# Kernel tuning notes

Hardware: AMD Instinct MI355X
Metric: run time of the kernel (lower is better)

The kernel has to match this reference:

```python
import jax, jax.numpy as jnp
import numpy as np
from jax import lax

EPS = 1e-5
ALPHA = 100.0

def leaky_relu(x):
    return jnp.where(x >= 0, x, 0.2 * x)

def instance_norm(x):
    # per-sample, per-channel over (H, W), affine=False, eps=1e-5
    m = jnp.mean(x, axis=(2, 3), keepdims=True)
    v = jnp.var(x, axis=(2, 3), keepdims=True)
    return (x - m) / jnp.sqrt(v + EPS)

def conv2d(x, W, b, stride=1):
    y = lax.conv_general_dilated(x, W, (stride, stride), 'VALID',
                                 dimension_numbers=('NCHW', 'OIHW', 'NCHW'))
    return y + b[None, :, None, None]

def leaky_conv(x, W, b, pad, stride):
    # ReflectionPad2d(pad) -> Conv2d(pad=0) -> InstanceNorm -> LeakyReLU(0.2)
    if pad > 0:
        x = jnp.pad(x, ((0, 0), (0, 0), (pad, pad), (pad, pad)), mode='reflect')
    y = conv2d(x, W, b, stride)
    return leaky_relu(instance_norm(y))

def up2x_align_corners(x):
    # nn.UpsamplingBilinear2d(scale_factor=2) == bilinear with align_corners=True
    n, c, H, W = x.shape
    def coords(S):
        pos = jnp.arange(2 * S, dtype=x.dtype) * (S - 1) / (2 * S - 1)
        i0 = jnp.floor(pos).astype(jnp.int32)
        i1 = jnp.minimum(i0 + 1, S - 1)
        return i0, i1, pos - i0
    i0, i1, fh = coords(H)
    x = x[:, :, i0, :] * (1 - fh)[None, None, :, None] + x[:, :, i1, :] * fh[None, None, :, None]
    j0, j1, fw = coords(W)
    x = x[:, :, :, j0] * (1 - fw) + x[:, :, :, j1] * fw
    return x

def upsample_block(x, W, b):
    x = up2x_align_corners(x)
    # Conv2d(3,3,k=3,s=1,p=1) uses ZERO padding (plain nn.Conv2d padding arg)
    x = jnp.pad(x, ((0, 0), (0, 0), (1, 1), (1, 1)))
    return leaky_relu(instance_norm(conv2d(x, W, b)))

def cal_correlation(fa, fb, alpha):
    n, c, h, w = fa.shape
    fa = fa - jnp.mean(fa, axis=(2, 3), keepdims=True)
    fb = fb - jnp.mean(fb, axis=(2, 3), keepdims=True)
    fa = fa.reshape(n, c, h * w)
    fb = fb.reshape(n, c, h * w)
    fa = fa / (jnp.linalg.norm(fa, axis=1, keepdims=True) + EPS)
    fb = fb / (jnp.linalg.norm(fb, axis=1, keepdims=True) + EPS)
    energy = jnp.einsum('ncp,ncq->npq', fb, fa) * alpha  # [n, hw_b, hw_a]
    return jax.nn.softmax(energy, axis=1)

def setup_inputs() -> dict:
    key = jax.random.key(0)
    ks = jax.random.split(key, 16)
    C = 256
    d = {
        'fa_raw': jax.random.normal(ks[0], (2, C, 64, 64), jnp.float32),
        'fb_raw': jax.random.normal(ks[1], (2, C, 64, 64), jnp.float32),
        'fc_raw': jax.random.normal(ks[2], (2, 3, 256, 256), jnp.float32),
        'Wa': jax.random.normal(ks[3], (C // 4, C, 1, 1), jnp.float32) * 0.05,
        'ba': jnp.zeros((C // 4,), jnp.float32),
        'Wb': jax.random.normal(ks[4], (C // 4, C, 1, 1), jnp.float32) * 0.05,
        'bb': jnp.zeros((C // 4,), jnp.float32),
        'Wc1': jax.random.normal(ks[5], (3, 3, 3, 3), jnp.float32) * 0.2,
        'bc1': jnp.zeros((3,), jnp.float32),
        'Wc2': jax.random.normal(ks[6], (3, 3, 3, 3), jnp.float32) * 0.2,
        'bc2': jnp.zeros((3,), jnp.float32),
        'Wu1': jax.random.normal(ks[7], (3, 3, 3, 3), jnp.float32) * 0.2,
        'bu1': jnp.zeros((3,), jnp.float32),
        'Wu2': jax.random.normal(ks[8], (3, 3, 3, 3), jnp.float32) * 0.2,
        'bu2': jnp.zeros((3,), jnp.float32),
    }
    return d

def reference(fa_raw, fb_raw, fc_raw, Wa, ba, Wb, bb, Wc1, bc1, Wc2, bc2, Wu1, bu1, Wu2, bu2):
    fa = leaky_conv(fa_raw, Wa, ba, pad=0, stride=1)          # [n, 64, 64, 64]
    fb = leaky_conv(fb_raw, Wb, bb, pad=0, stride=1)
    fc = leaky_conv(fc_raw, Wc1, bc1, pad=1, stride=2)        # [n, 3, 128, 128]
    fc = leaky_conv(fc, Wc2, bc2, pad=1, stride=2)            # [n, 3, 64, 64]
    corr_ab_T = cal_correlation(fa, fb, ALPHA)                # [n, 4096, 4096]
    n, c, h, w = fc.shape
    fc_warp = jnp.einsum('ncp,npq->ncq', fc.reshape(n, c, h * w), corr_ab_T)
    fc_warp = fc_warp.reshape(n, c, h, w)
    fc_warp = upsample_block(fc_warp, Wu1, bu1)               # [n, 3, 128, 128]
    fc_warp = upsample_block(fc_warp, Wu2, bu2)               # [n, 3, 256, 256]
    return fc_warp, corr_ab_T
```

## Files before the change

kernel.cpp:

```cpp
#include <hip/hip_runtime.h>
#include <math.h>

#define EPS 1e-5f

typedef short short8 __attribute__((ext_vector_type(8)));
typedef __bf16 bf16x8 __attribute__((ext_vector_type(8)));
typedef float f32x4  __attribute__((ext_vector_type(4)));

__device__ __forceinline__ float lrelu(float x){ return x >= 0.f ? x : 0.2f*x; }

__device__ __forceinline__ short f2bf_s(float x){
    unsigned u = __float_as_uint(x);
    unsigned r = (u + 0x7FFFu + ((u >> 16) & 1u)) >> 16;
    return (short)r;
}
__device__ __forceinline__ float bfs2f(short h){
    return __uint_as_float(((unsigned)(unsigned short)h) << 16);
}

__device__ __forceinline__ f32x4 mfma16(bf16x8 a, bf16x8 b, f32x4 c){
    return __builtin_amdgcn_mfma_f32_16x16x32_bf16(a, b, c, 0, 0, 0);
}

__global__ __launch_bounds__(256,2) void feat_conv(
    const float* __restrict__ fa_raw, const float* __restrict__ fb_raw,
    const float* __restrict__ Wa, const float* __restrict__ Wb,
    const float* __restrict__ ba, const float* __restrict__ bb,
    float* __restrict__ Y, float* __restrict__ FSUM)
{
    __shared__ float wS[256*65];
    __shared__ float xS[16*64];

    int blk = blockIdx.x;
    int pch = blk & 63, n = (blk>>6)&1, side = blk>>7;
    int p0 = pch*64;
    const float* x    = (side ? fb_raw : fa_raw) + (size_t)n*256*4096 + p0;
    const float* W    = side ? Wb : Wa;
    const float* bias = side ? bb : ba;
    int tid = threadIdx.x;

    #pragma unroll
    for (int it=0; it<64; it++){
        int idx = it*256 + tid;
        int co = idx >> 8, ci = idx & 255;
        wS[ci*65 + co] = W[idx];
    }

    int pl = tid & 63, cog = tid >> 6;
    float acc[16];
    #pragma unroll
    for (int j=0;j<16;j++) acc[j] = 0.f;

    for (int cb=0; cb<16; cb++){
        __syncthreads();
        #pragma unroll
        for (int it=0; it<4; it++){
            int idx = it*256 + tid;
            int cl = idx >> 6, pp = idx & 63;
            xS[idx] = x[(size_t)(cb*16+cl)*4096 + pp];
        }
        __syncthreads();
        #pragma unroll
        for (int cl=0; cl<16; cl++){
            float xr = xS[cl*64 + pl];
            const float* wr = &wS[(cb*16+cl)*65 + cog*16];
            #pragma unroll
            for (int j=0;j<16;j++) acc[j] = fmaf(xr, wr[j], acc[j]);
        }
    }

    int pair = side*2 + n;
    #pragma unroll
    for (int j=0;j<16;j++){
        acc[j] += bias[cog*16+j];
        float v = acc[j], v2 = v*v;
        #pragma unroll
        for (int off=1; off<64; off<<=1){
            v  += __shfl_xor(v,  off);
            v2 += __shfl_xor(v2, off);
        }
        if (pl == 0){
            atomicAdd(&FSUM[(pair*64 + cog*16 + j)*2],   v);
            atomicAdd(&FSUM[(pair*64 + cog*16 + j)*2+1], v2);
        }
    }

    float* yr = Y + ((size_t)pair*4096 + p0 + pl)*64 + cog*16;
    #pragma unroll
    for (int j4=0;j4<4;j4++)
        *(float4*)(yr + j4*4) = make_float4(acc[j4*4],acc[j4*4+1],acc[j4*4+2],acc[j4*4+3]);
}

__global__ __launch_bounds__(256) void feat_apply(
    float* __restrict__ Y, const float* __restrict__ FSUM, float* __restrict__ M2SUM)
{
    __shared__ float red[256];
    int tid = threadIdx.x;
    size_t base = (size_t)blockIdx.x*4096;
    int pair = (int)(base >> 18);
    int co = tid & 63;
    int ch = pair*64 + co;
    float m   = FSUM[ch*2]   * (1.f/4096.f);
    float var = FSUM[ch*2+1] * (1.f/4096.f) - m*m;
    float inv = rsqrtf(var + EPS);
    float asum = 0.f;
    #pragma unroll
    for (int it=0; it<16; it++){
        size_t idx = base + it*256 + tid;
        float y2 = lrelu((Y[idx]-m)*inv);
        Y[idx] = y2;
        asum += y2;
    }
    red[tid] = asum; __syncthreads();
    if (tid < 64)
        atomicAdd(&M2SUM[pair*64 + tid], red[tid]+red[tid+64]+red[tid+128]+red[tid+192]);
}

__global__ void feat_finish(const float* __restrict__ Y, const float* __restrict__ M2SUM,
                            short* __restrict__ PK)
{
    int r = blockIdx.x*256 + threadIdx.x;
    int pair = r >> 12;
    int p = r & 4095;
    const float4* m4 = (const float4*)(M2SUM + pair*64);
    const float4* r4 = (const float4*)(Y + (size_t)r*64);
    float s = 0.f;
    float4 v[16];
    #pragma unroll
    for (int i=0;i<16;i++){
        float4 t = r4[i], mm = m4[i];
        t.x -= mm.x*(1.f/4096.f); t.y -= mm.y*(1.f/4096.f);
        t.z -= mm.z*(1.f/4096.f); t.w -= mm.w*(1.f/4096.f);
        v[i] = t;
        s += t.x*t.x + t.y*t.y + t.z*t.z + t.w*t.w;
    }
    float inv = 1.f/(sqrtf(s)+EPS);
    #pragma unroll
    for (int i=0;i<16;i++){ v[i].x*=inv; v[i].y*=inv; v[i].z*=inv; v[i].w*=inv; }

    int qb = p >> 7, rr = p & 127, g = rr >> 4, rl = rr & 15;
    short* blk = PK + (((size_t)pair*32 + qb) << 14);
    #pragma unroll
    for (int c=0;c<8;c++){
        float x[8] = {v[2*c].x, v[2*c].y, v[2*c].z, v[2*c].w,
                      v[2*c+1].x, v[2*c+1].y, v[2*c+1].z, v[2*c+1].w};
        short8 h, l;
        #pragma unroll
        for (int j=0;j<8;j++){
            short hh = f2bf_s(x[j]);
            h[j] = hh;
            l[j] = f2bf_s(x[j] - bfs2f(hh));
        }
        int idx = g*128 + c*16 + rl;
        *(short8*)(blk + idx*8)        = h;
        *(short8*)(blk + 8192 + idx*8) = l;
    }
}

template<int STRIDE, bool REFLECT>
__global__ void conv3_kernel(const float* __restrict__ in_, int H, int Wd,
                             const float* __restrict__ wgt,
                             const float* __restrict__ bias,
                             float* __restrict__ out, float* __restrict__ sums)
{
    int oH = (H-1)/STRIDE + 1, oW = (Wd-1)/STRIDE + 1;
    int tid = threadIdx.x;
    size_t idx = (size_t)blockIdx.x*256 + tid;
    int ow = (int)(idx % oW); size_t t = idx / oW;
    int oh = (int)(t % oH); t /= oH;
    int co = (int)(t % 3); int n = (int)(t/3);
    float w[27];
    #pragma unroll
    for (int i=0;i<27;i++) w[i] = wgt[co*27 + i];
    float acc = bias[co];
    #pragma unroll
    for (int ci=0;ci<3;ci++){
        size_t base = ((size_t)(n*3+ci))*H*Wd;
        #pragma unroll
        for (int kh=0;kh<3;kh++){
            int ih = oh*STRIDE + kh - 1;
            if (REFLECT) ih = ih<0 ? -ih : (ih>=H ? 2*H-2-ih : ih);
            #pragma unroll
            for (int kw=0;kw<3;kw++){
                int iw = ow*STRIDE + kw - 1;
                if (REFLECT) iw = iw<0 ? -iw : (iw>=Wd ? 2*Wd-2-iw : iw);
                bool ok = REFLECT || (ih>=0 && ih<H && iw>=0 && iw<Wd);
                if (ok) acc += w[(ci*3+kh)*3+kw] * in_[base + (size_t)ih*Wd + iw];
            }
        }
    }
    out[idx] = acc;
    __shared__ float red[256];
    red[tid] = acc; __syncthreads();
    for (int o=128;o>0;o>>=1){ if(tid<o) red[tid]+=red[tid+o]; __syncthreads(); }
    float blockSum = red[0]; __syncthreads();
    red[tid] = acc*acc; __syncthreads();
    for (int o=128;o>0;o>>=1){ if(tid<o) red[tid]+=red[tid+o]; __syncthreads(); }
    if (tid==0){
        int pair = n*3+co;
        atomicAdd(&sums[pair*2],   blockSum);
        atomicAdd(&sums[pair*2+1], red[0]);
    }
}

template<int H>
__global__ __launch_bounds__(256) void upconv3_kernel(
    const float* __restrict__ in_, const float* __restrict__ wgt,
    const float* __restrict__ bias, float* __restrict__ out,
    float* __restrict__ sums)
{
    const int oH = 2*H;
    int tid = threadIdx.x;
    size_t idx = (size_t)blockIdx.x*256 + tid;
    int ow = (int)(idx % oH); size_t t = idx / oH;
    int oh = (int)(t % oH); t /= oH;
    int co = (int)(t % 3); int n = (int)(t/3);

    float w[27];
    #pragma unroll
    for (int i=0;i<27;i++) w[i] = wgt[co*27 + i];

    int i0[3], i1[3], j0[3], j1[3];
    float fh[3], fw[3];
    bool vh[3], vw[3];
    #pragma unroll
    for (int k=0;k<3;k++){
        int ih = oh + k - 1;
        vh[k] = (ih>=0 && ih<oH);
        int ihc = vh[k] ? ih : 0;
        float ph = (float)ihc * (float)(H-1) / (float)(oH-1);
        i0[k] = (int)ph; i1[k] = min(i0[k]+1, H-1); fh[k] = ph - (float)i0[k];
        int iw = ow + k - 1;
        vw[k] = (iw>=0 && iw<oH);
        int iwc = vw[k] ? iw : 0;
        float pw = (float)iwc * (float)(H-1) / (float)(oH-1);
        j0[k] = (int)pw; j1[k] = min(j0[k]+1, H-1); fw[k] = pw - (float)j0[k];
    }

    float acc = bias[co];
    #pragma unroll
    for (int ci=0;ci<3;ci++){
        const float* p = in_ + ((size_t)(n*3+ci))*H*H;
        #pragma unroll
        for (int kh=0;kh<3;kh++){
            if (!vh[kh]) continue;
            const float* r0 = p + (size_t)i0[kh]*H;
            const float* r1 = p + (size_t)i1[kh]*H;
            #pragma unroll
            for (int kw=0;kw<3;kw++){
                if (!vw[kw]) continue;
                float v00=r0[j0[kw]], v01=r0[j1[kw]];
                float v10=r1[j0[kw]], v11=r1[j1[kw]];
                float v0 = v00 + (v01-v00)*fw[kw];
                float v1 = v10 + (v11-v10)*fw[kw];
                float u  = v0 + (v1-v0)*fh[kh];
                acc += w[(ci*3+kh)*3+kw] * u;
            }
        }
    }
    out[idx] = acc;
    __shared__ float red[256];
    red[tid] = acc; __syncthreads();
    for (int o=128;o>0;o>>=1){ if(tid<o) red[tid]+=red[tid+o]; __syncthreads(); }
    float blockSum = red[0]; __syncthreads();
    red[tid] = acc*acc; __syncthreads();
    for (int o=128;o>0;o>>=1){ if(tid<o) red[tid]+=red[tid+o]; __syncthreads(); }
    if (tid==0){
        int pair = n*3+co;
        atomicAdd(&sums[pair*2],   blockSum);
        atomicAdd(&sums[pair*2+1], red[0]);
    }
}

__global__ void inapply_kernel(const float* __restrict__ in, const float* __restrict__ sums,
                               int planeSize, float cntInv, float* __restrict__ out)
{
    size_t idx = (size_t)blockIdx.x*256 + threadIdx.x;
    int pair = (int)(idx / planeSize);
    float m = sums[pair*2]*cntInv;
    float v = sums[pair*2+1]*cntInv - m*m;
    float inv = rsqrtf(v + EPS);
    out[idx] = lrelu((in[idx]-m)*inv);
}

template<int PASS>
__global__ __launch_bounds__(256,2) void corr_mfma(
    const short* __restrict__ PK,
    float* __restrict__ corr, float* __restrict__ SSUM,
    const float* __restrict__ fc, float* __restrict__ WARP)
{
    __shared__ short lds[32768];

    int blk = blockIdx.x;
    int qb = blk & 31, pb = (blk >> 5) & 31, n = blk >> 10;
    int tid = threadIdx.x;

    const short* pkB = PK + (((size_t)(2+n)*32 + pb) << 14);
    const short* pkA = PK + (((size_t)( n )*32 + qb) << 14);
    #pragma unroll
    for (int it=0; it<16; it++){
        int cid = it*256 + tid;
        int side = cid >> 11;
        int off  = (cid & 2047)*8;
        short8 vv = *(const short8*)((side ? pkA : pkB) + off);
        *(short8*)(lds + side*16384 + off) = vv;
    }
    __syncthreads();

    int wave = tid >> 6, lane = tid & 63;
    int wp = wave >> 1, wq = wave & 1;
    int quad = lane >> 4, l16 = lane & 15;

    f32x4 acc[4][4];
    #pragma unroll
    for (int pt=0;pt<4;pt++)
        #pragma unroll
        for (int qt=0;qt<4;qt++)
            acc[pt][qt] = (f32x4){0.f,0.f,0.f,0.f};

    #pragma unroll
    for (int kc=0;kc<2;kc++){
        int cc = kc*4 + quad;
        bf16x8 Ah[4], Al[4], Bh[4], Bl[4];
        #pragma unroll
        for (int t4=0;t4<4;t4++){
            int offA = (((wp*4+t4)*8 + cc)*16 + l16)*8;
            Ah[t4] = (bf16x8)(*(const short8*)(lds + offA));
            Al[t4] = (bf16x8)(*(const short8*)(lds + 8192 + offA));
            int offB = 16384 + (((wq*4+t4)*8 + cc)*16 + l16)*8;
            Bh[t4] = (bf16x8)(*(const short8*)(lds + offB));
            Bl[t4] = (bf16x8)(*(const short8*)(lds + 8192 + offB));
        }
        #pragma unroll
        for (int pt=0;pt<4;pt++)
            #pragma unroll
            for (int qt=0;qt<4;qt++){
                acc[pt][qt] = mfma16(Ah[pt], Bh[qt], acc[pt][qt]);
                acc[pt][qt] = mfma16(Ah[pt], Bl[qt], acc[pt][qt]);
                acc[pt][qt] = mfma16(Al[pt], Bh[qt], acc[pt][qt]);
            }
    }

    if (PASS == 0){
        float colsum[4] = {0.f,0.f,0.f,0.f};
        #pragma unroll
        for (int pt=0;pt<4;pt++)
            #pragma unroll
            for (int qt=0;qt<4;qt++)
                #pragma unroll
                for (int i=0;i<4;i++)
                    colsum[qt] += __expf(fmaf(acc[pt][qt][i], 100.f, -64.f));
        #pragma unroll
        for (int qt=0;qt<4;qt++){
            float v = colsum[qt];
            v += __shfl_xor(v, 16);
            v += __shfl_xor(v, 32);
            if (lane < 16)
                atomicAdd(&SSUM[n*4096 + qb*128 + wq*64 + qt*16 + lane], v);
        }
    } else {
        float inv4[4];
        int qoff = n*4096 + qb*128 + wq*64 + l16;
        #pragma unroll
        for (int qt=0;qt<4;qt++) inv4[qt] = 1.f / SSUM[qoff + qt*16];
        float wa0[4]={0,0,0,0}, wa1[4]={0,0,0,0}, wa2[4]={0,0,0,0};
        const float* fcb = fc + (size_t)n*12288;
        float* corrN = corr + (size_t)n*4096*4096;
        #pragma unroll
        for (int pt=0;pt<4;pt++){
            #pragma unroll
            for (int i=0;i<4;i++){
                int p = pb*128 + wp*64 + pt*16 + quad*4 + i;
                float f0 = fcb[p], f1 = fcb[4096+p], f2 = fcb[8192+p];
                float* rowp = corrN + (size_t)p*4096 + qb*128 + wq*64 + l16;
                #pragma unroll
                for (int qt=0;qt<4;qt++){
                    float u = __expf(fmaf(acc[pt][qt][i], 100.f, -64.f)) * inv4[qt];
                    __builtin_nontemporal_store(u, &rowp[qt*16]);
                    wa0[qt] += f0*u; wa1[qt] += f1*u; wa2[qt] += f2*u;
                }
            }
        }
        #pragma unroll
        for (int qt=0;qt<4;qt++){
            float v0 = wa0[qt], v1 = wa1[qt], v2 = wa2[qt];
            v0 += __shfl_xor(v0,16); v0 += __shfl_xor(v0,32);
            v1 += __shfl_xor(v1,16); v1 += __shfl_xor(v1,32);
            v2 += __shfl_xor(v2,16); v2 += __shfl_xor(v2,32);
            if (lane < 16){
                int q = qb*128 + wq*64 + qt*16 + lane;
                atomicAdd(&WARP[(size_t)n*12288 +        q], v0);
                atomicAdd(&WARP[(size_t)n*12288 + 4096 + q], v1);
                atomicAdd(&WARP[(size_t)n*12288 + 8192 + q], v2);
            }
        }
    }
}

extern "C" void kernel_launch(void* const* d_in, const int* in_sizes, int n_in,
                              void* d_out, int out_size, void* d_ws, size_t ws_size,
                              hipStream_t stream)
{
    const float* fa_raw = (const float*)d_in[0];
    const float* fb_raw = (const float*)d_in[1];
    const float* fc_raw = (const float*)d_in[2];
    const float* Wa  = (const float*)d_in[3];
    const float* ba  = (const float*)d_in[4];
    const float* Wb  = (const float*)d_in[5];
    const float* bb  = (const float*)d_in[6];
    const float* Wc1 = (const float*)d_in[7];
    const float* bc1 = (const float*)d_in[8];
    const float* Wc2 = (const float*)d_in[9];
    const float* bc2 = (const float*)d_in[10];
    const float* Wu1 = (const float*)d_in[11];
    const float* bu1 = (const float*)d_in[12];
    const float* Wu2 = (const float*)d_in[13];
    const float* bu2 = (const float*)d_in[14];

    float* ws    = (float*)d_ws;
    float* FEAT  = ws;
    float* CONV1 = FEAT  + 1048576;
    float* FC64  = CONV1 + 98304;
    float* CONV2 = FC64  + 24576;
    float* CONV3 = CONV2 + 98304;
    float* SSUM  = CONV3 + 393216;
    float* SUMS  = SSUM  + 8192;
    float* FSUM  = SUMS  + 48;
    float* M2SUM = FSUM  + 512;
    float* WARP  = M2SUM + 256;
    short* PK    = (short*)(WARP + 24576);

    float* out_fc   = (float*)d_out;
    float* out_corr = out_fc + 393216;

    hipMemsetAsync(SSUM, 0, (size_t)(8192 + 48 + 512 + 256 + 24576)*sizeof(float), stream);

    feat_conv<<<256,256,0,stream>>>(fa_raw, fb_raw, Wa, Wb, ba, bb, FEAT, FSUM);
    feat_apply<<<256,256,0,stream>>>(FEAT, FSUM, M2SUM);
    feat_finish<<<64,256,0,stream>>>(FEAT, M2SUM, PK);

    conv3_kernel<2,true><<<384,256,0,stream>>>(fc_raw, 256,256, Wc1, bc1, CONV1, SUMS+0);
    inapply_kernel<<<384,256,0,stream>>>(CONV1, SUMS+0, 16384, 1.f/16384.f, CONV1);
    conv3_kernel<2,true><<<96,256,0,stream>>>(CONV1, 128,128, Wc2, bc2, FC64, SUMS+12);
    inapply_kernel<<<96,256,0,stream>>>(FC64, SUMS+12, 4096, 1.f/4096.f, FC64);

    corr_mfma<0><<<2048,256,0,stream>>>(PK, out_corr, SSUM, FC64, WARP);
    corr_mfma<1><<<2048,256,0,stream>>>(PK, out_corr, SSUM, FC64, WARP);

    upconv3_kernel<64><<<384,256,0,stream>>>(WARP, Wu1, bu1, CONV2, SUMS+24);
    inapply_kernel<<<384,256,0,stream>>>(CONV2, SUMS+24, 16384, 1.f/16384.f, CONV2);

    upconv3_kernel<128><<<1536,256,0,stream>>>(CONV2, Wu2, bu2, CONV3, SUMS+36);
    inapply_kernel<<<1536,256,0,stream>>>(CONV3, SUMS+36, 65536, 1.f/65536.f, out_fc);
}
```

Baseline: 365.3 us.

## Fuse pre- and post-correlation stages into persistent kernels with grid barriers

Merges the feature 1x1 conv, instance-norm apply, centering and normalization/packing, and the fc conv chain into a single persistent kernel. That kernel synchronizes through software grid barriers on a global counter, and the FEAT intermediate round trip through memory goes away. The separate normalize passes are folded into the consumer convolutions and the corr kernel, and the two upsample convs plus the final apply become one barrier-synchronized kernel. This cuts launch count and memory traffic. In exchange it depends on every block being co-resident (512 blocks at 2 per CU, 768 at 3 per CU), or the barriers deadlock, and it adds spin-wait cost.

```diff
diff --git a/kernel.cpp b/kernel.cpp
--- a/kernel.cpp
+++ b/kernel.cpp
@@ -22,150 +22,28 @@
     return __builtin_amdgcn_mfma_f32_16x16x32_bf16(a, b, c, 0, 0, 0);
 }
 
-__global__ __launch_bounds__(256,2) void feat_conv(
-    const float* __restrict__ fa_raw, const float* __restrict__ fb_raw,
-    const float* __restrict__ Wa, const float* __restrict__ Wb,
-    const float* __restrict__ ba, const float* __restrict__ bb,
-    float* __restrict__ Y, float* __restrict__ FSUM)
-{
-    __shared__ float wS[256*65];
-    __shared__ float xS[16*64];
-
-    int blk = blockIdx.x;
-    int pch = blk & 63, n = (blk>>6)&1, side = blk>>7;
-    int p0 = pch*64;
-    const float* x    = (side ? fb_raw : fa_raw) + (size_t)n*256*4096 + p0;
-    const float* W    = side ? Wb : Wa;
-    const float* bias = side ? bb : ba;
-    int tid = threadIdx.x;
-
-    #pragma unroll
-    for (int it=0; it<64; it++){
-        int idx = it*256 + tid;
-        int co = idx >> 8, ci = idx & 255;
-        wS[ci*65 + co] = W[idx];
-    }
-
-    int pl = tid & 63, cog = tid >> 6;
-    float acc[16];
-    #pragma unroll
-    for (int j=0;j<16;j++) acc[j] = 0.f;
-
-    for (int cb=0; cb<16; cb++){
-        __syncthreads();
-        #pragma unroll
-        for (int it=0; it<4; it++){
-            int idx = it*256 + tid;
-            int cl = idx >> 6, pp = idx & 63;
-            xS[idx] = x[(size_t)(cb*16+cl)*4096 + pp];
-        }
-        __syncthreads();
-        #pragma unroll
-        for (int cl=0; cl<16; cl++){
-            float xr = xS[cl*64 + pl];
-            const float* wr = &wS[(cb*16+cl)*65 + cog*16];
-            #pragma unroll
-            for (int j=0;j<16;j++) acc[j] = fmaf(xr, wr[j], acc[j]);
-        }
-    }
-
-    int pair = side*2 + n;
-    #pragma unroll
-    for (int j=0;j<16;j++){
-        acc[j] += bias[cog*16+j];
-        float v = acc[j], v2 = v*v;
-        #pragma unroll
-        for (int off=1; off<64; off<<=1){
-            v  += __shfl_xor(v,  off);
-            v2 += __shfl_xor(v2, off);
-        }
-        if (pl == 0){
-            atomicAdd(&FSUM[(pair*64 + cog*16 + j)*2],   v);
-            atomicAdd(&FSUM[(pair*64 + cog*16 + j)*2+1], v2);
-        }
-    }
-
-    float* yr = Y + ((size_t)pair*4096 + p0 + pl)*64 + cog*16;
-    #pragma unroll
-    for (int j4=0;j4<4;j4++)
-        *(float4*)(yr + j4*4) = make_float4(acc[j4*4],acc[j4*4+1],acc[j4*4+2],acc[j4*4+3]);
-}
-
-__global__ __launch_bounds__(256) void feat_apply(
-    float* __restrict__ Y, const float* __restrict__ FSUM, float* __restrict__ M2SUM)
-{
-    __shared__ float red[256];
-    int tid = threadIdx.x;
-    size_t base = (size_t)blockIdx.x*4096;
-    int pair = (int)(base >> 18);
-    int co = tid & 63;
-    int ch = pair*64 + co;
-    float m   = FSUM[ch*2]   * (1.f/4096.f);
-    float var = FSUM[ch*2+1] * (1.f/4096.f) - m*m;
-    float inv = rsqrtf(var + EPS);
-    float asum = 0.f;
-    #pragma unroll
-    for (int it=0; it<16; it++){
-        size_t idx = base + it*256 + tid;
-        float y2 = lrelu((Y[idx]-m)*inv);
-        Y[idx] = y2;
-        asum += y2;
-    }
-    red[tid] = asum; __syncthreads();
-    if (tid < 64)
-        atomicAdd(&M2SUM[pair*64 + tid], red[tid]+red[tid+64]+red[tid+128]+red[tid+192]);
-}
-
-__global__ void feat_finish(const float* __restrict__ Y, const float* __restrict__ M2SUM,
-                            short* __restrict__ PK)
-{
-    int r = blockIdx.x*256 + threadIdx.x;
-    int pair = r >> 12;
-    int p = r & 4095;
-    const float4* m4 = (const float4*)(M2SUM + pair*64);
-    const float4* r4 = (const float4*)(Y + (size_t)r*64);
-    float s = 0.f;
-    float4 v[16];
-    #pragma unroll
-    for (int i=0;i<16;i++){
-        float4 t = r4[i], mm = m4[i];
-        t.x -= mm.x*(1.f/4096.f); t.y -= mm.y*(1.f/4096.f);
-        t.z -= mm.z*(1.f/4096.f); t.w -= mm.w*(1.f/4096.f);
-        v[i] = t;
-        s += t.x*t.x + t.y*t.y + t.z*t.z + t.w*t.w;
-    }
-    float inv = 1.f/(sqrtf(s)+EPS);
-    #pragma unroll
-    for (int i=0;i<16;i++){ v[i].x*=inv; v[i].y*=inv; v[i].z*=inv; v[i].w*=inv; }
-
-    int qb = p >> 7, rr = p & 127, g = rr >> 4, rl = rr & 15;
-    short* blk = PK + (((size_t)pair*32 + qb) << 14);
-    #pragma unroll
-    for (int c=0;c<8;c++){
-        float x[8] = {v[2*c].x, v[2*c].y, v[2*c].z, v[2*c].w,
-                      v[2*c+1].x, v[2*c+1].y, v[2*c+1].z, v[2*c+1].w};
-        short8 h, l;
-        #pragma unroll
-        for (int j=0;j<8;j++){
-            short hh = f2bf_s(x[j]);
-            h[j] = hh;
-            l[j] = f2bf_s(x[j] - bfs2f(hh));
-        }
-        int idx = g*128 + c*16 + rl;
-        *(short8*)(blk + idx*8)        = h;
-        *(short8*)(blk + 8192 + idx*8) = l;
-    }
-}
-
-template<int STRIDE, bool REFLECT>
-__global__ void conv3_kernel(const float* __restrict__ in_, int H, int Wd,
-                             const float* __restrict__ wgt,
-                             const float* __restrict__ bias,
-                             float* __restrict__ out, float* __restrict__ sums)
+__device__ __forceinline__ void gbar(unsigned* cnt, unsigned target){
+    __syncthreads();
+    if (threadIdx.x == 0){
+        __threadfence();
+        __hip_atomic_fetch_add(cnt, 1u, __ATOMIC_ACQ_REL, __HIP_MEMORY_SCOPE_AGENT);
+        while (__hip_atomic_load(cnt, __ATOMIC_ACQUIRE, __HIP_MEMORY_SCOPE_AGENT) < target)
+            __builtin_amdgcn_s_sleep(8);
+        __threadfence();
+    }
+    __syncthreads();
+}
+
+template<int STRIDE, bool REFLECT, bool NORM>
+__device__ __forceinline__ void conv3_unit(
+    int u, const float* __restrict__ in_, int H, int Wd,
+    const float* __restrict__ wgt, const float* __restrict__ bias,
+    const float* __restrict__ nsum, float cntInv,
+    float* __restrict__ out, float* __restrict__ sums, float* red)
 {
     int oH = (H-1)/STRIDE + 1, oW = (Wd-1)/STRIDE + 1;
     int tid = threadIdx.x;
-    size_t idx = (size_t)blockIdx.x*256 + tid;
+    size_t idx = (size_t)u*256 + tid;
     int ow = (int)(idx % oW); size_t t = idx / oW;
     int oh = (int)(t % oH); t /= oH;
     int co = (int)(t % 3); int n = (int)(t/3);
@@ -175,6 +53,13 @@
     float acc = bias[co];
     #pragma unroll
     for (int ci=0;ci<3;ci++){
+        float mm = 0.f, iv = 0.f;
+        if (NORM){
+            int pr = n*3+ci;
+            float m_ = nsum[pr*2]*cntInv;
+            float v_ = nsum[pr*2+1]*cntInv - m_*m_;
+            mm = m_; iv = rsqrtf(v_ + EPS);
+        }
         size_t base = ((size_t)(n*3+ci))*H*Wd;
         #pragma unroll
         for (int kh=0;kh<3;kh++){
@@ -185,12 +70,15 @@
                 int iw = ow*STRIDE + kw - 1;
                 if (REFLECT) iw = iw<0 ? -iw : (iw>=Wd ? 2*Wd-2-iw : iw);
                 bool ok = REFLECT || (ih>=0 && ih<H && iw>=0 && iw<Wd);
-                if (ok) acc += w[(ci*3+kh)*3+kw] * in_[base + (size_t)ih*Wd + iw];
+                if (ok){
+                    float val = in_[base + (size_t)ih*Wd + iw];
+                    if (NORM) val = lrelu((val-mm)*iv);
+                    acc += w[(ci*3+kh)*3+kw] * val;
+                }
             }
         }
     }
     out[idx] = acc;
-    __shared__ float red[256];
     red[tid] = acc; __syncthreads();
     for (int o=128;o>0;o>>=1){ if(tid<o) red[tid]+=red[tid+o]; __syncthreads(); }
     float blockSum = red[0]; __syncthreads();
@@ -201,17 +89,19 @@
         atomicAdd(&sums[pair*2],   blockSum);
         atomicAdd(&sums[pair*2+1], red[0]);
     }
-}
-
-template<int H>
-__global__ __launch_bounds__(256) void upconv3_kernel(
-    const float* __restrict__ in_, const float* __restrict__ wgt,
-    const float* __restrict__ bias, float* __restrict__ out,
-    float* __restrict__ sums)
+    __syncthreads();
+}
+
+template<int H, bool NORM>
+__device__ __forceinline__ void upconv3_unit(
+    int u, const float* __restrict__ in_,
+    const float* __restrict__ wgt, const float* __restrict__ bias,
+    const float* __restrict__ nsum, float cntInv,
+    float* __restrict__ out, float* __restrict__ sums, float* red)
 {
     const int oH = 2*H;
     int tid = threadIdx.x;
-    size_t idx = (size_t)blockIdx.x*256 + tid;
+    size_t idx = (size_t)u*256 + tid;
     int ow = (int)(idx % oH); size_t t = idx / oH;
     int oh = (int)(t % oH); t /= oH;
     int co = (int)(t % 3); int n = (int)(t/3);
@@ -240,6 +130,13 @@
     float acc = bias[co];
     #pragma unroll
     for (int ci=0;ci<3;ci++){
+        float mm = 0.f, iv = 0.f;
+        if (NORM){
+            int pr = n*3+ci;
+            float m_ = nsum[pr*2]*cntInv;
+            float v_ = nsum[pr*2+1]*cntInv - m_*m_;
+            mm = m_; iv = rsqrtf(v_ + EPS);
+        }
         const float* p = in_ + ((size_t)(n*3+ci))*H*H;
         #pragma unroll
         for (int kh=0;kh<3;kh++){
@@ -251,15 +148,18 @@
                 if (!vw[kw]) continue;
                 float v00=r0[j0[kw]], v01=r0[j1[kw]];
                 float v10=r1[j0[kw]], v11=r1[j1[kw]];
+                if (NORM){
+                    v00 = lrelu((v00-mm)*iv); v01 = lrelu((v01-mm)*iv);
+                    v10 = lrelu((v10-mm)*iv); v11 = lrelu((v11-mm)*iv);
+                }
                 float v0 = v00 + (v01-v00)*fw[kw];
                 float v1 = v10 + (v11-v10)*fw[kw];
-                float u  = v0 + (v1-v0)*fh[kh];
-                acc += w[(ci*3+kh)*3+kw] * u;
+                float uu = v0 + (v1-v0)*fh[kh];
+                acc += w[(ci*3+kh)*3+kw] * uu;
             }
         }
     }
     out[idx] = acc;
-    __shared__ float red[256];
     red[tid] = acc; __syncthreads();
     for (int o=128;o>0;o>>=1){ if(tid<o) red[tid]+=red[tid+o]; __syncthreads(); }
     float blockSum = red[0]; __syncthreads();
@@ -270,24 +170,177 @@
         atomicAdd(&sums[pair*2],   blockSum);
         atomicAdd(&sums[pair*2+1], red[0]);
     }
-}
-
-__global__ void inapply_kernel(const float* __restrict__ in, const float* __restrict__ sums,
-                               int planeSize, float cntInv, float* __restrict__ out)
+    __syncthreads();
+}
+
+__global__ __launch_bounds__(256,2) void combo_kernel(
+    const float* __restrict__ fa_raw, const float* __restrict__ fb_raw,
+    const float* __restrict__ Wa, const float* __restrict__ Wb,
+    const float* __restrict__ ba, const float* __restrict__ bb,
+    const float* __restrict__ fc_raw,
+    const float* __restrict__ Wc1, const float* __restrict__ bc1,
+    const float* __restrict__ Wc2, const float* __restrict__ bc2,
+    float* __restrict__ CONV1, float* __restrict__ FC64,
+    float* __restrict__ FSUM, float* __restrict__ M2SUM,
+    float* __restrict__ SUMS, short* __restrict__ PK, unsigned* __restrict__ BAR)
 {
-    size_t idx = (size_t)blockIdx.x*256 + threadIdx.x;
-    int pair = (int)(idx / planeSize);
-    float m = sums[pair*2]*cntInv;
-    float v = sums[pair*2+1]*cntInv - m*m;
-    float inv = rsqrtf(v + EPS);
-    out[idx] = lrelu((in[idx]-m)*inv);
+    __shared__ float sh[17664];
+
+    int blk = blockIdx.x, tid = threadIdx.x;
+
+    if (blk < 256){
+        int pch = blk & 63, n = (blk>>6)&1, side = blk>>7;
+        int p0 = pch*64;
+        const float* x    = (side ? fb_raw : fa_raw) + (size_t)n*256*4096 + p0;
+        const float* W    = side ? Wb : Wa;
+        const float* bias = side ? bb : ba;
+        float* wS = sh;
+        float* xS = sh + 16640;
+
+        #pragma unroll
+        for (int it=0; it<64; it++){
+            int idx = it*256 + tid;
+            int co = idx >> 8, ci = idx & 255;
+            wS[ci*65 + co] = W[idx];
+        }
+
+        int pl = tid & 63, cog = tid >> 6;
+        float acc[16];
+        #pragma unroll
+        for (int j=0;j<16;j++) acc[j] = 0.f;
+
+        for (int cb=0; cb<16; cb++){
+            __syncthreads();
+            #pragma unroll
+            for (int it=0; it<4; it++){
+                int idx = it*256 + tid;
+                int cl = idx >> 6, pp = idx & 63;
+                xS[idx] = x[(size_t)(cb*16+cl)*4096 + pp];
+            }
+            __syncthreads();
+            #pragma unroll
+            for (int cl=0; cl<16; cl++){
+                float xr = xS[cl*64 + pl];
+                const float* wr = &wS[(cb*16+cl)*65 + cog*16];
+                #pragma unroll
+                for (int j=0;j<16;j++) acc[j] = fmaf(xr, wr[j], acc[j]);
+            }
+        }
+
+        int pair = side*2 + n;
+        #pragma unroll
+        for (int j=0;j<16;j++){
+            acc[j] += bias[cog*16+j];
+            float v = acc[j], v2 = v*v;
+            #pragma unroll
+            for (int off=1; off<64; off<<=1){
+                v  += __shfl_xor(v,  off);
+                v2 += __shfl_xor(v2, off);
+            }
+            if (pl == 0){
+                atomicAdd(&FSUM[(pair*64 + cog*16 + j)*2],   v);
+                atomicAdd(&FSUM[(pair*64 + cog*16 + j)*2+1], v2);
+            }
+        }
+
+        gbar(BAR, 512);
+
+        #pragma unroll
+        for (int j=0;j<16;j++){
+            int ch = pair*64 + cog*16 + j;
+            float m   = FSUM[ch*2]   * (1.f/4096.f);
+            float var = FSUM[ch*2+1] * (1.f/4096.f) - m*m;
+            float inv = rsqrtf(var + EPS);
+            acc[j] = lrelu((acc[j]-m)*inv);
+        }
+        #pragma unroll
+        for (int j=0;j<16;j++){
+            float v = acc[j];
+            #pragma unroll
+            for (int off=1; off<64; off<<=1) v += __shfl_xor(v, off);
+            if (pl == 0) atomicAdd(&M2SUM[pair*64 + cog*16 + j], v);
+        }
+
+        gbar(BAR, 1024);
+
+        float tch[16];
+        float s = 0.f;
+        #pragma unroll
+        for (int j=0;j<16;j++){
+            float tt = acc[j] - M2SUM[pair*64 + cog*16 + j]*(1.f/4096.f);
+            tch[j] = tt;
+            s += tt*tt;
+        }
+        sh[tid] = s; __syncthreads();
+        float tot = sh[pl] + sh[64+pl] + sh[128+pl] + sh[192+pl];
+        float inv = 1.f/(sqrtf(tot)+EPS);
+
+        int qb = pch >> 1, g = (pch&1)*4 + (pl>>4), rl = pl & 15;
+        short* pblk = PK + (((size_t)pair*32 + qb) << 14);
+        #pragma unroll
+        for (int c2=0;c2<2;c2++){
+            short8 h, l;
+            #pragma unroll
+            for (int j=0;j<8;j++){
+                float xv = tch[c2*8+j]*inv;
+                short hh = f2bf_s(xv);
+                h[j] = hh;
+                l[j] = f2bf_s(xv - bfs2f(hh));
+            }
+            int idx = g*128 + (cog*2+c2)*16 + rl;
+            *(short8*)(pblk + idx*8)        = h;
+            *(short8*)(pblk + 8192 + idx*8) = l;
+        }
+    } else {
+        int cb = blk - 256;
+        conv3_unit<2,true,false>(cb, fc_raw, 256,256, Wc1, bc1, nullptr, 0.f,
+                                 CONV1, SUMS+0, sh);
+        if (cb < 128)
+            conv3_unit<2,true,false>(cb+256, fc_raw, 256,256, Wc1, bc1, nullptr, 0.f,
+                                     CONV1, SUMS+0, sh);
+        gbar(BAR, 512);
+        if (cb < 96)
+            conv3_unit<2,true,true>(cb, CONV1, 128,128, Wc2, bc2, SUMS+0, 1.f/16384.f,
+                                    FC64, SUMS+12, sh);
+        gbar(BAR, 1024);
+    }
+}
+
+__global__ __launch_bounds__(256,3) void upchain_kernel(
+    const float* __restrict__ WARP,
+    const float* __restrict__ Wu1, const float* __restrict__ bu1,
+    const float* __restrict__ Wu2, const float* __restrict__ bu2,
+    float* __restrict__ CONV2, float* __restrict__ CONV3,
+    float* __restrict__ SUMS, float* __restrict__ out_fc, unsigned* __restrict__ BAR)
+{
+    __shared__ float red[256];
+    int b = blockIdx.x, tid = threadIdx.x;
+
+    if (b < 384)
+        upconv3_unit<64,false>(b, WARP, Wu1, bu1, nullptr, 0.f, CONV2, SUMS+24, red);
+    gbar(BAR, 768);
+
+    upconv3_unit<128,true>(b,     CONV2, Wu2, bu2, SUMS+24, 1.f/16384.f, CONV3, SUMS+36, red);
+    upconv3_unit<128,true>(b+768, CONV2, Wu2, bu2, SUMS+24, 1.f/16384.f, CONV3, SUMS+36, red);
+    gbar(BAR, 1536);
+
+    #pragma unroll
+    for (int k=0;k<2;k++){
+        size_t idx = (size_t)(b + k*768)*256 + tid;
+        int pair = (int)(idx >> 16);
+        float m   = SUMS[36 + pair*2]   * (1.f/65536.f);
+        float var = SUMS[36 + pair*2+1] * (1.f/65536.f) - m*m;
+        float inv = rsqrtf(var + EPS);
+        out_fc[idx] = lrelu((CONV3[idx]-m)*inv);
+    }
 }
 
 template<int PASS>
 __global__ __launch_bounds__(256,2) void corr_mfma(
     const short* __restrict__ PK,
     float* __restrict__ corr, float* __restrict__ SSUM,
-    const float* __restrict__ fc, float* __restrict__ WARP)
+    const float* __restrict__ FC64, const float* __restrict__ fsums,
+    float* __restrict__ WARP)
 {
     __shared__ short lds[32768];
 
@@ -363,15 +416,26 @@
         int qoff = n*4096 + qb*128 + wq*64 + l16;
         #pragma unroll
         for (int qt=0;qt<4;qt++) inv4[qt] = 1.f / SSUM[qoff + qt*16];
+
+        float fm[3], fiv[3];
+        #pragma unroll
+        for (int c=0;c<3;c++){
+            float m_ = fsums[(n*3+c)*2]   * (1.f/4096.f);
+            float v_ = fsums[(n*3+c)*2+1] * (1.f/4096.f) - m_*m_;
+            fm[c] = m_; fiv[c] = rsqrtf(v_ + EPS);
+        }
+
         float wa0[4]={0,0,0,0}, wa1[4]={0,0,0,0}, wa2[4]={0,0,0,0};
-        const float* fcb = fc + (size_t)n*12288;
+        const float* fcb = FC64 + (size_t)n*12288;
         float* corrN = corr + (size_t)n*4096*4096;
         #pragma unroll
         for (int pt=0;pt<4;pt++){
             #pragma unroll
             for (int i=0;i<4;i++){
                 int p = pb*128 + wp*64 + pt*16 + quad*4 + i;
-                float f0 = fcb[p], f1 = fcb[4096+p], f2 = fcb[8192+p];
+                float f0 = lrelu((fcb[p]      -fm[0])*fiv[0]);
+                float f1 = lrelu((fcb[4096+p] -fm[1])*fiv[1]);
+                float f2 = lrelu((fcb[8192+p] -fm[2])*fiv[2]);
                 float* rowp = corrN + (size_t)p*4096 + qb*128 + wq*64 + l16;
                 #pragma unroll
                 for (int qt=0;qt<4;qt++){
@@ -418,8 +482,7 @@
     const float* bu2 = (const float*)d_in[14];
 
     float* ws    = (float*)d_ws;
-    float* FEAT  = ws;
-    float* CONV1 = FEAT  + 1048576;
+    float* CONV1 = ws;
     float* FC64  = CONV1 + 98304;
     float* CONV2 = FC64  + 24576;
     float* CONV3 = CONV2 + 98304;
@@ -428,28 +491,21 @@
     float* FSUM  = SUMS  + 48;
     float* M2SUM = FSUM  + 512;
     float* WARP  = M2SUM + 256;
-    short* PK    = (short*)(WARP + 24576);
+    unsigned* BAR = (unsigned*)(WARP + 24576);
+    short* PK    = (short*)(WARP + 24576 + 16);
 
     float* out_fc   = (float*)d_out;
     float* out_corr = out_fc + 393216;
 
-    hipMemsetAsync(SSUM, 0, (size_t)(8192 + 48 + 512 + 256 + 24576)*sizeof(float), stream);
-
-    feat_conv<<<256,256,0,stream>>>(fa_raw, fb_raw, Wa, Wb, ba, bb, FEAT, FSUM);
-    feat_apply<<<256,256,0,stream>>>(FEAT, FSUM, M2SUM);
-    feat_finish<<<64,256,0,stream>>>(FEAT, M2SUM, PK);
-
-    conv3_kernel<2,true><<<384,256,0,stream>>>(fc_raw, 256,256, Wc1, bc1, CONV1, SUMS+0);
-    inapply_kernel<<<384,256,0,stream>>>(CONV1, SUMS+0, 16384, 1.f/16384.f, CONV1);
-    conv3_kernel<2,true><<<96,256,0,stream>>>(CONV1, 128,128, Wc2, bc2, FC64, SUMS+12);
-    inapply_kernel<<<96,256,0,stream>>>(FC64, SUMS+12, 4096, 1.f/4096.f, FC64);
-
-    corr_mfma<0><<<2048,256,0,stream>>>(PK, out_corr, SSUM, FC64, WARP);
-    corr_mfma<1><<<2048,256,0,stream>>>(PK, out_corr, SSUM, FC64, WARP);
-
-    upconv3_kernel<64><<<384,256,0,stream>>>(WARP, Wu1, bu1, CONV2, SUMS+24);
-    inapply_kernel<<<384,256,0,stream>>>(CONV2, SUMS+24, 16384, 1.f/16384.f, CONV2);
-
-    upconv3_kernel<128><<<1536,256,0,stream>>>(CONV2, Wu2, bu2, CONV3, SUMS+36);
-    inapply_kernel<<<1536,256,0,stream>>>(CONV3, SUMS+36, 65536, 1.f/65536.f, out_fc);
-}
+    hipMemsetAsync(SSUM, 0, (size_t)(8192 + 48 + 512 + 256 + 24576 + 16)*sizeof(float), stream);
+
+    combo_kernel<<<512,256,0,stream>>>(fa_raw, fb_raw, Wa, Wb, ba, bb,
+                                       fc_raw, Wc1, bc1, Wc2, bc2,
+                                       CONV1, FC64, FSUM, M2SUM, SUMS, PK, BAR);
+
+    corr_mfma<0><<<2048,256,0,stream>>>(PK, out_corr, SSUM, FC64, SUMS+12, WARP);
+    corr_mfma<1><<<2048,256,0,stream>>>(PK, out_corr, SSUM, FC64, SUMS+12, WARP);
+
+    upchain_kernel<<<768,256,0,stream>>>(WARP, Wu1, bu1, Wu2, bu2,
+                                         CONV2, CONV3, SUMS, out_fc, BAR+1);
+}
```

After: 849.4 us. +132.5%, slower.
